# Performance work log

Hardware: AMD Instinct MI355X
Metric: run time of the kernel (lower is better)

Reference implementation:

```python
import jax, jax.numpy as jnp
import numpy as np

B, L, H, N = 50, 1024, 512, 512
DT = 1e-3          # step from source
N_DEQ = 8          # fixed-point iterations for the implicit (DEQ) layer
EPS = 1e-5


def setup_inputs():
    key = jax.random.key(0)
    ks = jax.random.split(key, 8)
    s = lambda k, shape: jax.random.normal(k, shape, jnp.float32) * 0.02
    return dict(
        x=jax.random.normal(ks[0], (B, L, 1), jnp.float32),
        W_emb=s(ks[1], (1, H)), b_emb=jnp.zeros((H,), jnp.float32),
        C_re=s(ks[2], (6, H, N)), C_im=s(ks[3], (6, H, N)),
        D=jnp.ones((6, H), jnp.float32),
        ln_g=jnp.ones((6, H), jnp.float32), ln_b=jnp.zeros((6, H), jnp.float32),
        W_feed=s(ks[4], (H, H)), b_feed=jnp.zeros((H,), jnp.float32),
        W_fc=s(ks[5], (H, 10)), b_fc=jnp.zeros((10,), jnp.float32),
    )


def _kernels(C_re, C_im):
    # S4D-Lin init for A (shared across channels in this untrained reference):
    # A_n = -1/2 + i*pi*n. ZOH discretization with step DT.
    n = jnp.arange(N)
    A = -0.5 + 1j * jnp.pi * n                       # [N]
    dA = jnp.exp(DT * A)                              # [N]
    dB = (dA - 1.0) / A                               # [N] (B = 1)
    l = jnp.arange(L)
    V = jnp.exp(DT * A[:, None] * l[None, :])         # [N, L] Vandermonde dA^l
    C = C_re.astype(jnp.complex64) + 1j * C_im.astype(jnp.complex64)  # [6,H,N]
    K = 2.0 * jnp.real(jnp.einsum('khn,nl->khl', C * dB, V))          # [6,H,L]
    return K.astype(jnp.float32)


def _conv(u, K):
    # causal convolution of u [B,L,H] with per-channel kernel K [H,L]
    Uf = jnp.fft.rfft(u, n=2 * L, axis=1)             # [B, L+1, H]
    Kf = jnp.fft.rfft(K.T, n=2 * L, axis=0)           # [L+1, H]
    y = jnp.fft.irfft(Uf * Kf[None], n=2 * L, axis=1)[:, :L]
    return y


def _ln(x, g, b):
    m = jnp.mean(x, axis=-1, keepdims=True)
    v = jnp.var(x, axis=-1, keepdims=True)
    return (x - m) * jax.lax.rsqrt(v + EPS) * g + b


def _s4d_block(u, K, D, g, b, act, skip):
    v = _ln(u, g, b)
    y = act(_conv(v, K) + v * D)                      # SSM + skip-through D
    return y + u if skip else y


def _deq(x, Ks, Ds, gs, bs, W_feed, b_feed):
    # implicit layer: fixed-point of z = f(z; x), f = 3 stacked S4D blocks
    # + gelu + gelu feedforward, with input injection (skip=False, dropout=0)
    def f(z):
        h = z + x
        for i in range(3):
            h = _s4d_block(h, Ks[i], Ds[i], gs[i], bs[i], jnp.tanh, False)
        h = jax.nn.gelu(h)
        return jax.nn.gelu(h @ W_feed + b_feed)
    z = jnp.zeros_like(x)
    for _ in range(N_DEQ - 1):
        z = f(z)
    z_new = f(z)
    loss = jnp.mean((z_new - z) ** 2)                 # fixed-point residual
    return z_new, loss


def reference(x, W_emb, b_emb, C_re, C_im, D, ln_g, ln_b, W_feed, b_feed, W_fc, b_fc):
    K = _kernels(C_re, C_im)                          # [6,H,L]
    r = x @ W_emb + b_emb                             # [B,L,H]
    y = r
    for i in range(3):                                # 3 explicit S4D blocks
        y = _s4d_block(y, K[i], D[i], ln_g[i], ln_b[i], jnp.tanh, True)
    h, loss = _deq(y, K[3:], D[3:], ln_g[3:], ln_b[3:], W_feed, b_feed)
    logits = jnp.mean(h, axis=1) @ W_fc + b_fc        # [B,10]
    return logits, loss, h, jnp.int32(N_DEQ)
```

## Files before the change

### kernel.cpp

```cpp
#include <hip/hip_runtime.h>
#include <hip/hip_bf16.h>

typedef __hip_bfloat16 bf16;
typedef unsigned short u16;
typedef unsigned int u32;
typedef __attribute__((ext_vector_type(8))) short short8;
typedef __attribute__((ext_vector_type(4))) float f32x4;

#define B_ 50
#define L_ 1024
#define H_ 512
#define N_ 512
#define BL_ 51200
#define HBL_ 26214400
#define KROW_ 1088
#define PI_F 3.14159265358979323846f
#define MARK_BF16 0x3F803F80u
#define KRSW_ 1112
#define CONV_LDS_BYTES 151040

#define FF_RES 131072
#define FF_SB  140288
#define FF_RED 142336
#define FF2_LDS_BYTES 144384
#define WAB(kc,m,cb) ((((kc)<<13) + ((m)<<7)) + ((cb) ^ (((((m)^(kc))&7))<<4)))
#define YTB(kc,n,cb) (65536 + (((kc)<<13) + ((n)<<7)) + ((cb) ^ (((((n)&7)^((n)>>3)^(kc))&7)<<4)))

__device__ __forceinline__ float u2f(u16 u){ union{u32 i; float f;} v; v.i = ((u32)u)<<16; return v.f; }
__device__ __forceinline__ u16  f2u(float x){ bf16 b = __float2bfloat16(x); return *(u16*)&b; }

__device__ __forceinline__ float ld_in(const void* p, int i, bool bff){
  if (bff){ u16 v = ((const u16*)p)[i]; union{u32 a; float f;} u; u.a = ((u32)v)<<16; return u.f; }
  return ((const float*)p)[i];
}

__device__ __forceinline__ float tanh_f(float x){
  float ax = fabsf(x);
  float e = __expf(2.f*ax);
  float r = 1.f - 2.f/(e + 1.f);
  return copysignf(r, x);
}

__device__ __forceinline__ float gelu_f(float x){
  float t = tanh_f(0.7978845608028654f*(x + 0.044715f*x*x*x));
  return 0.5f*x*(1.0f + t);
}

__global__ __launch_bounds__(256) void kV(float* __restrict__ Vre, float* __restrict__ Vim){
  int idx = blockIdx.x*256 + threadIdx.x;
  int n = idx >> 10, l = idx & 1023;
  int ph = (n*l) % 2000;
  float ang = (float)ph * (PI_F/1000.f);
  float mag = expf(-5e-4f*(float)l);
  float s, c;
  sincosf(ang, &s, &c);
  Vre[idx] = mag*c;
  Vim[idx] = mag*s;
}

__global__ __launch_bounds__(256) void kX(const u32* __restrict__ mk,
                                          const void* __restrict__ Cre, const void* __restrict__ Cim,
                                          float* __restrict__ Xre, float* __restrict__ Xim){
  const bool bff = (*mk == MARK_BF16);
  int idx = blockIdx.x*256 + threadIdx.x;
  int n = idx & (N_-1);
  float ar = -0.5f, ai = PI_F*(float)n;
  float ex = expf(-5e-4f);
  float s, c;
  sincosf(1e-3f*ai, &s, &c);
  float dre = ex*c - 1.f;
  float dim = ex*s;
  float inv = 1.f/(ar*ar + ai*ai);
  float dBre = (dre*ar + dim*ai)*inv;
  float dBim = (dim*ar - dre*ai)*inv;
  float cr = ld_in(Cre, idx, bff), ci = ld_in(Cim, idx, bff);
  Xre[idx] = cr*dBre - ci*dBim;
  Xim[idx] = cr*dBim + ci*dBre;
}

__global__ __launch_bounds__(256) void kK(const float* __restrict__ Xre, const float* __restrict__ Xim,
                                          const float* __restrict__ Vre, const float* __restrict__ Vim,
                                          u16* __restrict__ Kbp){
  __shared__ float sxr[8*128], sxi[8*128];
  int kh0 = blockIdx.x*8;
  int l0 = blockIdx.y*512 + threadIdx.x;
  float accA[8], accB[8];
  #pragma unroll
  for (int t=0;t<8;++t){ accA[t]=0.f; accB[t]=0.f; }
  for (int nc=0; nc<4; ++nc){
    if (nc) __syncthreads();
    #pragma unroll
    for (int q=0;q<4;++q){
      int e = q*256 + threadIdx.x;
      int r = e >> 7, c = e & 127;
      sxr[e] = Xre[(kh0+r)*N_ + nc*128 + c];
      sxi[e] = Xim[(kh0+r)*N_ + nc*128 + c];
    }
    __syncthreads();
    for (int n4=0;n4<32;++n4){
      int nb = (nc*128 + n4*4)*L_ + l0;
      float vrA[4], viA[4], vrB[4], viB[4];
      #pragma unroll
      for (int k=0;k<4;++k){
        vrA[k] = Vre[nb + k*L_];       viA[k] = Vim[nb + k*L_];
        vrB[k] = Vre[nb + k*L_ + 256]; viB[k] = Vim[nb + k*L_ + 256];
      }
      #pragma unroll
      for (int t=0;t<8;++t){
        f32x4 xr = *(const f32x4*)&sxr[t*128 + n4*4];
        f32x4 xi = *(const f32x4*)&sxi[t*128 + n4*4];
        float a = accA[t], b = accB[t];
        #pragma unroll
        for (int k=0;k<4;++k){
          a += xr[k]*vrA[k] - xi[k]*viA[k];
          b += xr[k]*vrB[k] - xi[k]*viB[k];
        }
        accA[t] = a; accB[t] = b;
      }
    }
  }
  #pragma unroll
  for (int t=0;t<8;++t){
    Kbp[(kh0+t)*KROW_ + 64 + l0]       = f2u(2.f*accA[t]);
    Kbp[(kh0+t)*KROW_ + 64 + l0 + 256] = f2u(2.f*accB[t]);
  }
  if (blockIdx.y == 0 && threadIdx.x < 64){
    #pragma unroll
    for (int t=0;t<8;++t) Kbp[(kh0+t)*KROW_ + threadIdx.x] = 0;
  }
}

__global__ __launch_bounds__(256) void kWb(const u32* __restrict__ mk,
                                           const void* __restrict__ W, u16* __restrict__ Wbt){
  const bool bff = (*mk == MARK_BF16);
  int idx = blockIdx.x*256 + threadIdx.x;
  int k = idx >> 9, m = idx & 511;
  Wbt[m*512 + k] = f2u(ld_in(W, k*512 + m, bff));
}

__global__ __launch_bounds__(256) void kEmbed(const u32* __restrict__ mk,
                                              const void* __restrict__ x, const void* __restrict__ W,
                                              const void* __restrict__ be, u16* __restrict__ out){
  const bool bff = (*mk == MARK_BF16);
  int t = blockIdx.x*256 + threadIdx.x;
  int e = t*4;
  int h = e / BL_;
  int col = e - h*BL_;
  float w = ld_in(W, h, bff), bb = ld_in(be, h, bff);
  ushort4 o;
  o.x = f2u(ld_in(x, col+0, bff)*w + bb);
  o.y = f2u(ld_in(x, col+1, bff)*w + bb);
  o.z = f2u(ld_in(x, col+2, bff)*w + bb);
  o.w = f2u(ld_in(x, col+3, bff)*w + bb);
  *(ushort4*)(out + e) = o;
}

__global__ __launch_bounds__(256) void kZero(uint4* __restrict__ Z, float* __restrict__ lossAcc){
  int t = blockIdx.x*256 + threadIdx.x;
  Z[t] = make_uint4(0u,0u,0u,0u);
  if (t == 0) *lossAcc = 0.f;
}

__global__ __launch_bounds__(256) void kLN2(const u32* __restrict__ mk,
                                            const u16* __restrict__ U, const u16* __restrict__ U2,
                                            const void* __restrict__ g, const void* __restrict__ bb,
                                            int off, u16* __restrict__ Vout){
  const bool bff = (*mk == MARK_BF16);
  __shared__ float rs[32][64], rq[32][64], ms[64], rr[64], gs[512], bs[512];
  int c8 = threadIdx.x & 7;
  int ty = threadIdx.x >> 3;
  int colb = blockIdx.x*64 + c8*8;
  for (int i = threadIdx.x; i < 512; i += 256){
    gs[i] = ld_in(g, off+i, bff);
    bs[i] = ld_in(bb, off+i, bff);
  }
  float s8[8], q8[8];
  #pragma unroll
  for (int j=0;j<8;++j){ s8[j]=0.f; q8[j]=0.f; }
  for (int p=0;p<16;++p){
    int h = ty + p*32;
    uint4 uv = *(const uint4*)(U + (size_t)h*BL_ + colb);
    const u16* pu = (const u16*)&uv;
    float xv[8];
    #pragma unroll
    for (int j=0;j<8;++j) xv[j] = u2f(pu[j]);
    if (U2){
      uint4 uv2 = *(const uint4*)(U2 + (size_t)h*BL_ + colb);
      const u16* p2 = (const u16*)&uv2;
      #pragma unroll
      for (int j=0;j<8;++j) xv[j] += u2f(p2[j]);
    }
    #pragma unroll
    for (int j=0;j<8;++j){ s8[j] += xv[j]; q8[j] += xv[j]*xv[j]; }
  }
  *(f32x4*)&rs[ty][c8*8]   = (f32x4){s8[0],s8[1],s8[2],s8[3]};
  *(f32x4*)&rs[ty][c8*8+4] = (f32x4){s8[4],s8[5],s8[6],s8[7]};
  *(f32x4*)&rq[ty][c8*8]   = (f32x4){q8[0],q8[1],q8[2],q8[3]};
  *(f32x4*)&rq[ty][c8*8+4] = (f32x4){q8[4],q8[5],q8[6],q8[7]};
  __syncthreads();
  if (threadIdx.x < 64){
    int c = threadIdx.x;
    float st = 0.f, qt = 0.f;
    #pragma unroll 8
    for (int t2=0;t2<32;++t2){ st += rs[t2][c]; qt += rq[t2][c]; }
    float mean = st*(1.f/512.f);
    float var  = qt*(1.f/512.f) - mean*mean;
    ms[c] = mean;
    rr[c] = rsqrtf(var + 1e-5f);
  }
  __syncthreads();
  float mean8[8], rstd8[8];
  #pragma unroll
  for (int j=0;j<8;++j){ mean8[j] = ms[c8*8+j]; rstd8[j] = rr[c8*8+j]; }
  for (int p=0;p<16;++p){
    int h = ty + p*32;
    uint4 uv = *(const uint4*)(U + (size_t)h*BL_ + colb);
    const u16* pu = (const u16*)&uv;
    float xv[8];
    #pragma unroll
    for (int j=0;j<8;++j) xv[j] = u2f(pu[j]);
    if (U2){
      uint4 uv2 = *(const uint4*)(U2 + (size_t)h*BL_ + colb);
      const u16* p2 = (const u16*)&uv2;
      #pragma unroll
      for (int j=0;j<8;++j) xv[j] += u2f(p2[j]);
    }
    float gv = gs[h], bv = bs[h];
    union { uint4 v; u16 s[8]; } ob;
    #pragma unroll
    for (int j=0;j<8;++j) ob.s[j] = f2u((xv[j]-mean8[j])*rstd8[j]*gv + bv);
    *(uint4*)(Vout + (size_t)h*BL_ + colb) = ob.v;
  }
}

__global__ __launch_bounds__(512, 2) void kConvM(const u32* __restrict__ mk,
                                              const u16* __restrict__ V, const u16* __restrict__ Kb,
                                              const void* __restrict__ Dv, int dOff,
                                              const u16* __restrict__ U,
                                              u16* __restrict__ Y, int skip, int doGelu){
  extern __shared__ u16 lds[];
  u16* sV  = lds;
  u16* sKR = lds + 65536;
  u16* sKt = lds + 65536 + 8*KRSW_;
  const bool bff = (*mk == MARK_BF16);
  int h = blockIdx.x;
  int tid = threadIdx.x;
  const u16* Kbh = Kb + h*KROW_;
  for (int s = tid; s < 1088; s += 512) sKt[s] = Kbh[s];
  __syncthreads();
  #pragma unroll
  for (int p = 0; p < 8; ++p){
    for (int s = tid; s < KRSW_; s += 512){
      int idx = 1087 - s - p;
      sKR[p*KRSW_ + s] = (idx >= 0) ? sKt[idx] : (u16)0;
    }
  }
  {
    const u16* Vh = V + (size_t)h*(B_*L_);
    #pragma unroll
    for (int q = 0; q < 16; ++q){
      int chunk = q*512 + tid;
      int r = chunk >> 7;
      int c16 = chunk & 127;
      uint4 dval = *(const uint4*)(Vh + r*L_ + c16*8);
      u32 byte = ((u32)r << 11) + ((u32)c16 << 4);
      byte ^= ((u32)(r & 7) << 4);
      *(uint4*)((char*)sV + byte) = dval;
    }
  }
  __syncthreads();
  int wv = tid >> 6, lane = tid & 63;
  int nl = lane & 15, quad = lane >> 4;
  float Dh = ld_in(Dv, dOff + h, bff);
  #pragma unroll 1
  for (int cc = 0; cc < 2; ++cc){
    int c_out = cc ? (15 - wv) : wv;
    f32x4 acc[4][4];
    #pragma unroll
    for (int mt=0;mt<4;++mt){
      #pragma unroll
      for (int nt=0;nt<4;++nt) acc[mt][nt] = (f32x4){0.f,0.f,0.f,0.f};
    }
    for (int ci = 0; ci <= c_out; ++ci){
      int d = c_out - ci;
      short8 a0[4], a1[4], b0[4], b1[4];
      #pragma unroll
      for (int mt=0;mt<4;++mt){
        int r = mt*16 + nl;
        u32 msk = (u32)(r & 7) << 4;
        u32 base = ((u32)r << 11) + (u32)((ci*64 + quad*8) << 1);
        a0[mt] = *(const short8*)((const char*)sV + (base ^ msk));
        a1[mt] = *(const short8*)((const char*)sV + ((base + 64u) ^ msk));
      }
      #pragma unroll
      for (int nt=0;nt<4;++nt){
        int i = nt*16 + nl;
        int t0 = 1023 - d*64 - i + quad*8;
        const u16* bp = sKR + (t0 & 7)*KRSW_ + (t0 & ~7);
        b0[nt] = *(const short8*)bp;
        b1[nt] = *(const short8*)(bp + 32);
      }
      #pragma unroll
      for (int mt=0;mt<4;++mt){
        #pragma unroll
        for (int nt=0;nt<4;++nt){
          acc[mt][nt] = __builtin_amdgcn_mfma_f32_16x16x32_bf16(a0[mt], b0[nt], acc[mt][nt], 0,0,0);
          acc[mt][nt] = __builtin_amdgcn_mfma_f32_16x16x32_bf16(a1[mt], b1[nt], acc[mt][nt], 0,0,0);
        }
      }
    }
    #pragma unroll
    for (int mt=0;mt<4;++mt){
      #pragma unroll
      for (int reg=0;reg<4;++reg){
        int b = mt*16 + quad*4 + reg;
        if (b < B_){
          #pragma unroll
          for (int nt=0;nt<4;++nt){
            int col = c_out*64 + nt*16 + nl;
            u32 vb = (((u32)b << 11) + ((u32)col << 1)) ^ ((u32)(b & 7) << 4);
            float vv = u2f(*(const u16*)((const char*)sV + vb));
            size_t gi = (size_t)(h*B_ + b)*L_ + col;
            float y = tanh_f(acc[mt][nt][reg] + vv*Dh);
            if (skip) y += u2f(U[gi]);
            if (doGelu) y = gelu_f(y);
            Y[gi] = f2u(y);
          }
        }
      }
    }
  }
}

__global__ __launch_bounds__(512, 2) void kFF2(const u32* __restrict__ mk,
                                            const u16* __restrict__ Yin, const u16* __restrict__ Wbt,
                                            const void* __restrict__ bias, u16* __restrict__ Zout,
                                            const u16* __restrict__ Zold, float* __restrict__ lossAcc,
                                            int doLoss){
  extern __shared__ char ldsF[];
  u16* res  = (u16*)(ldsF + FF_RES);
  float* sb = (float*)(ldsF + FF_SB);
  float* red= (float*)(ldsF + FF_RED);
  const bool bff = (*mk == MARK_BF16);
  int n0g = blockIdx.x*64;
  int tid = threadIdx.x;

  sb[tid & 511] = ld_in(bias, tid & 511, bff);

  int rW = tid >> 3, kq = tid & 7;
  uint4 wreg[8];
  {
    const u16* wp = Wbt + (size_t)rW*512 + kq*64;
    #pragma unroll
    for (int i=0;i<8;++i) wreg[i] = *(const uint4*)(wp + i*8);
  }

  {
    int rY = tid >> 3, q3 = tid & 7;
    #pragma unroll
    for (int kc=0;kc<8;++kc){
      const u16* yp = Yin + (size_t)(kc*64 + rY)*BL_ + n0g + q3*8;
      uint4 v = *(const uint4*)yp;
      const u16* pv = (const u16*)&v;
      int nb = q3*8;
      #pragma unroll
      for (int j=0;j<8;++j) *(u16*)(ldsF + YTB(kc, nb+j, rY*2)) = pv[j];
    }
  }
  #pragma unroll
  for (int i=0;i<8;++i) *(uint4*)(ldsF + WAB(kq, rW, i*16)) = wreg[i];
  __syncthreads();

  int wv = tid >> 6, lane = tid & 63;
  int nl = lane & 15, quad = lane >> 4;
  int mt = wv >> 1, ntb = (wv & 1)*2;
  int mrow = mt*16 + nl;
  int nr0 = ntb*16 + nl, nr1 = nr0 + 16;
  {
    const u16* wp = Wbt + (size_t)64*512 + (size_t)rW*512 + kq*64;
    #pragma unroll
    for (int i=0;i<8;++i) wreg[i] = *(const uint4*)(wp + i*8);
  }

  float ls = 0.f;
  int frow = tid >> 3, fcol = (tid & 7)*8;

  #pragma unroll 1
  for (int mc=0; mc<8; ++mc){
    f32x4 acc0 = (f32x4){0.f,0.f,0.f,0.f};
    f32x4 acc1 = (f32x4){0.f,0.f,0.f,0.f};
    #pragma unroll
    for (int kc=0;kc<8;++kc){
      short8 a0  = *(const short8*)(ldsF + WAB(kc, mrow, quad*16));
      short8 a1  = *(const short8*)(ldsF + WAB(kc, mrow, 64 + quad*16));
      short8 b00 = *(const short8*)(ldsF + YTB(kc, nr0, quad*16));
      short8 b01 = *(const short8*)(ldsF + YTB(kc, nr0, 64 + quad*16));
      short8 b10 = *(const short8*)(ldsF + YTB(kc, nr1, quad*16));
      short8 b11 = *(const short8*)(ldsF + YTB(kc, nr1, 64 + quad*16));
      acc0 = __builtin_amdgcn_mfma_f32_16x16x32_bf16(a0, b00, acc0, 0,0,0);
      acc0 = __builtin_amdgcn_mfma_f32_16x16x32_bf16(a1, b01, acc0, 0,0,0);
      acc1 = __builtin_amdgcn_mfma_f32_16x16x32_bf16(a0, b10, acc1, 0,0,0);
      acc1 = __builtin_amdgcn_mfma_f32_16x16x32_bf16(a1, b11, acc1, 0,0,0);
    }
    #pragma unroll
    for (int reg=0;reg<4;++reg){
      int mloc = mt*16 + quad*4 + reg;
      float bv = sb[mc*64 + mloc];
      res[mloc*72 + ntb*16 + nl]      = f2u(gelu_f(acc0[reg] + bv));
      res[mloc*72 + ntb*16 + nl + 16] = f2u(gelu_f(acc1[reg] + bv));
    }
    __syncthreads();
    if (mc < 7){
      #pragma unroll
      for (int i=0;i<8;++i) *(uint4*)(ldsF + WAB(kq, rW, i*16)) = wreg[i];
    }
    {
      size_t zoff = (size_t)(mc*64 + frow)*BL_ + n0g + fcol;
      uint4 v = *(const uint4*)&res[frow*72 + fcol];
      if (doLoss){
        uint4 zo = *(const uint4*)(Zold + zoff);
        const u16* pv = (const u16*)&v;
        const u16* po = (const u16*)&zo;
        #pragma unroll
        for (int j=0;j<8;++j){ float d = u2f(pv[j]) - u2f(po[j]); ls += d*d; }
      }
      *(uint4*)(Zout + zoff) = v;
    }
    if (mc < 6){
      const u16* wp = Wbt + (size_t)(mc+2)*64*512 + (size_t)rW*512 + kq*64;
      #pragma unroll
      for (int i=0;i<8;++i) wreg[i] = *(const uint4*)(wp + i*8);
    }
    __syncthreads();
  }
  if (doLoss){
    red[tid] = ls;
    __syncthreads();
    for (int off=256; off>0; off>>=1){
      if (tid < off) red[tid] += red[tid+off];
      __syncthreads();
    }
    if (tid==0) atomicAdd(lossAcc, red[0]);
  }
}

__global__ void kScalars(const float* __restrict__ lossAcc, float* __restrict__ outp){
  if (threadIdx.x == 0 && blockIdx.x == 0){
    outp[500] = *lossAcc * (1.f/26214400.f);
    outp[26214901] = 8.0f;
  }
}

__global__ __launch_bounds__(256) void kTrans(const u16* __restrict__ Z, float* __restrict__ out){
  __shared__ u16 st[64][68];
  int b = blockIdx.z, h0 = blockIdx.y*64, l0 = blockIdx.x*64;
  int tid = threadIdx.x;
  int r = tid >> 2, q = tid & 3;
  const u16* src = Z + ((h0+r)*B_ + b)*L_ + l0 + q*16;
  #pragma unroll
  for (int c=0; c<4; ++c){
    ushort4 v = *(const ushort4*)(src + c*4);
    st[r][q*16 + c*4 + 0] = v.x;
    st[r][q*16 + c*4 + 1] = v.y;
    st[r][q*16 + c*4 + 2] = v.z;
    st[r][q*16 + c*4 + 3] = v.w;
  }
  __syncthreads();
  int i = tid & 63;
  int j0 = tid >> 6;
  for (int jj = j0; jj < 64; jj += 4){
    out[(size_t)(b*L_ + l0 + jj)*H_ + h0 + i] = u2f(st[i][jj]);
  }
}

__global__ __launch_bounds__(256) void kMeanL(const u16* __restrict__ Z, float* __restrict__ Hb){
  int lane = threadIdx.x & 63;
  int ridx = blockIdx.x*4 + (threadIdx.x >> 6);
  const u16* row = Z + (size_t)ridx*L_;
  float s = 0.f;
  for (int ii=lane; ii<L_; ii+=64) s += u2f(row[ii]);
  for (int off=32; off>0; off>>=1) s += __shfl_down(s, off, 64);
  if (lane==0){
    int ho = ridx / B_, b = ridx - ho*B_;
    Hb[b*H_ + ho] = s*(1.f/1024.f);
  }
}

__global__ __launch_bounds__(256) void kLogits(const u32* __restrict__ mk,
                                               const float* __restrict__ Hb, const void* __restrict__ Wfc,
                                               const void* __restrict__ bfc, float* __restrict__ outp){
  const bool bff = (*mk == MARK_BF16);
  int t = blockIdx.x*256 + threadIdx.x;
  if (t < 500){
    int b = t/10, c = t - (t/10)*10;
    float s = ld_in(bfc, c, bff);
    for (int ho=0; ho<H_; ++ho) s += Hb[b*H_+ho]*ld_in(Wfc, ho*10+c, bff);
    outp[t] = s;
  }
}

extern "C" void kernel_launch(void* const* d_in, const int* in_sizes, int n_in,
                              void* d_out, int out_size, void* d_ws, size_t ws_size,
                              hipStream_t stream) {
  (void)in_sizes; (void)n_in; (void)out_size; (void)ws_size;
  const void* x      = d_in[0];
  const void* W_emb  = d_in[1];
  const void* b_emb  = d_in[2];
  const void* C_re   = d_in[3];
  const void* C_im   = d_in[4];
  const void* Dp     = d_in[5];
  const void* ln_g   = d_in[6];
  const void* ln_b   = d_in[7];
  const void* W_feed = d_in[8];
  const void* b_feed = d_in[9];
  const void* W_fc   = d_in[10];
  const void* b_fc   = d_in[11];
  const u32* mk = (const u32*)d_in[5];
  float* outp = (float*)d_out;

  static int s_attr = 0;
  if (!s_attr){
    hipFuncSetAttribute(reinterpret_cast<const void*>(kConvM),
                        hipFuncAttributeMaxDynamicSharedMemorySize, CONV_LDS_BYTES);
    hipFuncSetAttribute(reinterpret_cast<const void*>(kFF2),
                        hipFuncAttributeMaxDynamicSharedMemorySize, FF2_LDS_BYTES);
    s_attr = 1;
  }

  u16* Kbp = (u16*)d_ws;
  u16* Zb  = Kbp + 6*H_*KROW_;
  u16* T1  = Zb + HBL_;
  u16* T2  = T1 + HBL_;
  float* Hbar = (float*)(T2 + HBL_);
  float* lossAcc = Hbar + 25600;
  u16* Wbt = (u16*)(Hbar + 25604);
  u16* X0  = (u16*)d_out;
  float* Vre = (float*)T1;
  float* Vim = Vre + N_*L_;
  float* Xre = Vim + N_*L_;
  float* Xim = Xre + 6*H_*N_;

  kV<<<2048, 256, 0, stream>>>(Vre, Vim);
  kX<<<6144, 256, 0, stream>>>(mk, C_re, C_im, Xre, Xim);
  kK<<<dim3(384,2), 256, 0, stream>>>(Xre, Xim, Vre, Vim, Kbp);
  kWb<<<1024, 256, 0, stream>>>(mk, W_feed, Wbt);

  kEmbed<<<25600, 256, 0, stream>>>(mk, x, W_emb, b_emb, X0);

  u16* cur = X0;
  u16* nxt = T2;
  for (int i=0;i<3;++i){
    kLN2<<<800,256,0,stream>>>(mk, cur, nullptr, ln_g, ln_b, i*H_, T1);
    kConvM<<<512, 512, CONV_LDS_BYTES, stream>>>(mk, T1, Kbp + i*H_*KROW_, Dp, i*H_, cur, nxt, 1, 0);
    u16* tmp = cur; cur = nxt; nxt = tmp;
  }
  u16* XINJ = cur;
  u16* BT   = nxt;

  kZero<<<12800, 256, 0, stream>>>((uint4*)Zb, lossAcc);
  for (int it=0; it<8; ++it){
    int last = (it == 7);
    kLN2<<<800,256,0,stream>>>(mk, Zb, XINJ, ln_g, ln_b, 3*H_, T1);
    kConvM<<<512, 512, CONV_LDS_BYTES, stream>>>(mk, T1, Kbp + 3*H_*KROW_, Dp, 3*H_, nullptr, BT, 0, 0);
    kLN2<<<800,256,0,stream>>>(mk, BT, nullptr, ln_g, ln_b, 4*H_, T1);
    kConvM<<<512, 512, CONV_LDS_BYTES, stream>>>(mk, T1, Kbp + 4*H_*KROW_, Dp, 4*H_, nullptr, BT, 0, 0);
    kLN2<<<800,256,0,stream>>>(mk, BT, nullptr, ln_g, ln_b, 5*H_, T1);
    kConvM<<<512, 512, CONV_LDS_BYTES, stream>>>(mk, T1, Kbp + 5*H_*KROW_, Dp, 5*H_, nullptr, BT, 0, 1);
    kFF2<<<800, 512, FF2_LDS_BYTES, stream>>>(mk, BT, Wbt, b_feed, Zb, Zb, lossAcc, last);
  }

  kMeanL<<<6400,256,0,stream>>>(Zb, Hbar);
  kScalars<<<1, 64, 0, stream>>>(lossAcc, outp);
  kTrans<<<dim3(16,8,50),256,0,stream>>>(Zb, outp + 501);
  kLogits<<<2,256,0,stream>>>(mk, Hbar, W_fc, b_fc, outp);
}
```

Baseline: 5.001 ms.

## Read FF weight fragments directly from global memory instead of staging in LDS

Measured after the change: 4.208 ms. -15.9%, faster.

```diff
diff --git a/kernel.cpp b/kernel.cpp
--- a/kernel.cpp
+++ b/kernel.cpp
@@ -19,12 +19,11 @@
 #define KRSW_ 1112
 #define CONV_LDS_BYTES 151040
 
-#define FF_RES 131072
-#define FF_SB  140288
-#define FF_RED 142336
-#define FF2_LDS_BYTES 144384
-#define WAB(kc,m,cb) ((((kc)<<13) + ((m)<<7)) + ((cb) ^ (((((m)^(kc))&7))<<4)))
-#define YTB(kc,n,cb) (65536 + (((kc)<<13) + ((n)<<7)) + ((cb) ^ (((((n)&7)^((n)>>3)^(kc))&7)<<4)))
+#define FF_RES 65536
+#define FF_SB  74752
+#define FF_RED 76800
+#define FF2_LDS_BYTES 78848
+#define YTB(kc,n,cb) ((((kc)<<13) + ((n)<<7)) + ((cb) ^ (((((n)&7)^((n)>>3)^(kc))&7)<<4)))
 
 __device__ __forceinline__ float u2f(u16 u){ union{u32 i; float f;} v; v.i = ((u32)u)<<16; return v.f; }
 __device__ __forceinline__ u16  f2u(float x){ bf16 b = __float2bfloat16(x); return *(u16*)&b; }
@@ -332,7 +331,7 @@
   }
 }
 
-__global__ __launch_bounds__(512, 2) void kFF2(const u32* __restrict__ mk,
+__global__ __launch_bounds__(512, 4) void kFF2(const u32* __restrict__ mk,
                                             const u16* __restrict__ Yin, const u16* __restrict__ Wbt,
                                             const void* __restrict__ bias, u16* __restrict__ Zout,
                                             const u16* __restrict__ Zold, float* __restrict__ lossAcc,
@@ -347,14 +346,6 @@
 
   sb[tid & 511] = ld_in(bias, tid & 511, bff);
 
-  int rW = tid >> 3, kq = tid & 7;
-  uint4 wreg[8];
-  {
-    const u16* wp = Wbt + (size_t)rW*512 + kq*64;
-    #pragma unroll
-    for (int i=0;i<8;++i) wreg[i] = *(const uint4*)(wp + i*8);
-  }
-
   {
     int rY = tid >> 3, q3 = tid & 7;
     #pragma unroll
@@ -367,8 +358,6 @@
       for (int j=0;j<8;++j) *(u16*)(ldsF + YTB(kc, nb+j, rY*2)) = pv[j];
     }
   }
-  #pragma unroll
-  for (int i=0;i<8;++i) *(uint4*)(ldsF + WAB(kq, rW, i*16)) = wreg[i];
   __syncthreads();
 
   int wv = tid >> 6, lane = tid & 63;
@@ -376,11 +365,6 @@
   int mt = wv >> 1, ntb = (wv & 1)*2;
   int mrow = mt*16 + nl;
   int nr0 = ntb*16 + nl, nr1 = nr0 + 16;
-  {
-    const u16* wp = Wbt + (size_t)64*512 + (size_t)rW*512 + kq*64;
-    #pragma unroll
-    for (int i=0;i<8;++i) wreg[i] = *(const uint4*)(wp + i*8);
-  }
 
   float ls = 0.f;
   int frow = tid >> 3, fcol = (tid & 7)*8;
@@ -389,10 +373,11 @@
   for (int mc=0; mc<8; ++mc){
     f32x4 acc0 = (f32x4){0.f,0.f,0.f,0.f};
     f32x4 acc1 = (f32x4){0.f,0.f,0.f,0.f};
+    const u16* wrow = Wbt + (size_t)(mc*64 + mrow)*512 + quad*8;
     #pragma unroll
     for (int kc=0;kc<8;++kc){
-      short8 a0  = *(const short8*)(ldsF + WAB(kc, mrow, quad*16));
-      short8 a1  = *(const short8*)(ldsF + WAB(kc, mrow, 64 + quad*16));
+      short8 a0  = *(const short8*)(wrow + kc*64);
+      short8 a1  = *(const short8*)(wrow + kc*64 + 32);
       short8 b00 = *(const short8*)(ldsF + YTB(kc, nr0, quad*16));
       short8 b01 = *(const short8*)(ldsF + YTB(kc, nr0, 64 + quad*16));
       short8 b10 = *(const short8*)(ldsF + YTB(kc, nr1, quad*16));
@@ -410,10 +395,6 @@
       res[mloc*72 + ntb*16 + nl + 16] = f2u(gelu_f(acc1[reg] + bv));
     }
     __syncthreads();
-    if (mc < 7){
-      #pragma unroll
-      for (int i=0;i<8;++i) *(uint4*)(ldsF + WAB(kq, rW, i*16)) = wreg[i];
-    }
     {
       size_t zoff = (size_t)(mc*64 + frow)*BL_ + n0g + fcol;
       uint4 v = *(const uint4*)&res[frow*72 + fcol];
@@ -425,11 +406,6 @@
         for (int j=0;j<8;++j){ float d = u2f(pv[j]) - u2f(po[j]); ls += d*d; }
       }
       *(uint4*)(Zout + zoff) = v;
-    }
-    if (mc < 6){
-      const u16* wp = Wbt + (size_t)(mc+2)*64*512 + (size_t)rW*512 + kq*64;
-      #pragma unroll
-      for (int i=0;i<8;++i) wreg[i] = *(const uint4*)(wp + i*8);
     }
     __syncthreads();
   }
```
